# Performance work log

Measured on AMD Instinct MI355X. Metric: run time of the kernel, lower is better.

Reference implementation:

```python
import jax, jax.numpy as jnp
import numpy as np

N = 262144   # query points
M = 4096     # boundary points
D = 128      # d_model (m)
H = 4        # num_heads
HD = D // H  # head_dim = 32
L = 3        # num_layers
PI = float(np.pi)


def multi_feature_encoding(x):
    # x: [T, 2] -> [T, 30]; 15 fixed feature maps, hstacked
    feats = [
        x,
        x ** 2,
        (x - 1.5) ** 2,
        (x - 4.5) ** 2,
        jax.nn.sigmoid(x),
        jax.nn.sigmoid(x - 1.5),
        jax.nn.sigmoid(x - 4.5),
        x - 1.5,
        x - 4.5,
        jnp.sin(PI * x),
        jnp.cos(PI * x),
        jnp.sin(PI * x * 0.25),
        jnp.cos(PI * x * 0.25),
        jnp.sin(PI * x * 0.5),
        jnp.cos(PI * x * 0.5),
    ]
    return jnp.concatenate(feats, axis=-1)


def pos_encode(x, w, b):
    # w: [30, D], b: [D]
    return jnp.sin(multi_feature_encoding(x) @ w + b)


def setup_inputs() -> dict:
    key = jax.random.key(0)
    ks = jax.random.split(key, 24)
    s = 0.05

    def p(k, shape):
        return jax.random.normal(k, shape, dtype=jnp.float32) * s

    return {
        "query_pts": jax.random.normal(ks[0], (N, 2), dtype=jnp.float32),
        "boundary_pts": jax.random.normal(ks[1], (M, 2), dtype=jnp.float32),
        # positional encoders (query / boundary)
        "pe_w": p(ks[2], (30, D)), "pe_b": p(ks[3], (D,)),
        "bpe_w": p(ks[4], (30, D)), "bpe_b": p(ks[5], (D,)),
        # per-layer per-head q/k/v projections, stacked: [L, H, D, HD]
        "Wq": p(ks[6], (L, H, D, HD)), "bq": p(ks[7], (L, H, HD)),
        "Wk": p(ks[8], (L, H, D, HD)), "bk": p(ks[9], (L, H, HD)),
        "Wv": p(ks[10], (L, H, D, HD)), "bv": p(ks[11], (L, H, HD)),
        # attention out proj and FFN (two D->D linears) per layer
        "Wo": p(ks[12], (L, D, D)), "bo": p(ks[13], (L, D)),
        "W1": p(ks[14], (L, D, D)), "b1": p(ks[15], (L, D)),
        "W2": p(ks[16], (L, D, D)), "b2": p(ks[17], (L, D)),
        # final projector: D -> D//2 -> 3
        "pw1": p(ks[18], (D, D // 2)), "pb1": p(ks[19], (D // 2,)),
        "pw2": p(ks[20], (D // 2, 3)), "pb2": p(ks[21], (3,)),
    }


def reference(query_pts, boundary_pts, pe_w, pe_b, bpe_w, bpe_b,
              Wq, bq, Wk, bk, Wv, bv, Wo, bo, W1, b1, W2, b2,
              pw1, pb1, pw2, pb2):
    h = pos_encode(query_pts, pe_w, pe_b)[None]        # [1, N, D]
    b_enc = pos_encode(boundary_pts, bpe_w, bpe_b)[None]  # [1, M, D]

    for l in range(L):
        # batched per-head projections (equivalent to the per-head Linear loop)
        qh = jnp.einsum('btd,hde->bhte', h, Wq[l]) + bq[l][None, :, None, :]
        kh = jnp.einsum('btd,hde->bhte', b_enc, Wk[l]) + bk[l][None, :, None, :]
        vh = jnp.einsum('btd,hde->bhte', b_enc, Wv[l]) + bv[l][None, :, None, :]
        qh = qh ** 2  # squared feature map
        kh = kh ** 2
        kv_sum = jnp.einsum('bhnd,bhne->bhde', kh, vh)          # [1,H,HD,HD]
        z = 1.0 / (jnp.einsum('bhnd,bhd->bhn', qh, kh.sum(axis=2)) + 1e-6)
        attn = jnp.einsum('bhnd,bhde,bhn->bhne', qh, kv_sum, z)  # [1,H,N,HD]
        attn = attn.transpose(0, 2, 1, 3).reshape(1, -1, D)      # [1,N,D]
        attn = attn @ Wo[l] + bo[l]
        x = h + attn
        ff = jax.nn.gelu(x @ W1[l] + b1[l], approximate=False) @ W2[l] + b2[l]
        h = x + ff

    out = jax.nn.gelu(h @ pw1 + pb1, approximate=False) @ pw2 + pb2  # [1,N,3]
    return out[0]  # squeeze(0) -> [N, 3]
```

## Files before the change

kernel.cpp:

```cpp
#include <hip/hip_runtime.h>
#include <hip/hip_bf16.h>

__device__ __forceinline__ float b2f(unsigned short u) {
    return __uint_as_float(((unsigned)u) << 16);
}
__device__ __forceinline__ unsigned short f2b(float f) {
    __hip_bfloat16 h = __float2bfloat16(f);
    return *reinterpret_cast<unsigned short*>(&h);
}
__device__ __forceinline__ unsigned pk_bf16(float lo, float hi) {
    unsigned r;
    asm("v_cvt_pk_bf16_f32 %0, %1, %2" : "=v"(r) : "v"(lo), "v"(hi));
    return r;
}
__device__ __forceinline__ float sigm(float v) {
    return 1.f / (1.f + __expf(-v));
}
__device__ __forceinline__ float gelu_l(float x) {
    float x2 = x * x;
    float y2 = x * __builtin_fmaf(0.0713548163f, x2, 1.5957691216f);
    float e  = __expf(y2);
    float r  = __builtin_amdgcn_rcpf(e + 1.f);
    return x - x * r;
}

typedef __attribute__((ext_vector_type(8))) short s8v;
typedef __attribute__((ext_vector_type(4))) float f4v;

#define MFMA_BF16 __builtin_amdgcn_mfma_f32_16x16x32_bf16

__device__ __forceinline__ s8v mkfrag(unsigned a, unsigned b, unsigned c, unsigned d) {
    union { unsigned u[4]; s8v v; } x;
    x.u[0] = a; x.u[1] = b; x.u[2] = c; x.u[3] = d;
    return x.v;
}

__device__ __forceinline__ int fmap(int s) {
    return (s & ~31) | (((s >> 2) & 3) << 3) | (((s >> 4) & 1) << 2) | (s & 3);
}

__device__ __forceinline__ void make_feats(const unsigned short* __restrict__ qpts,
                                           int r, float* __restrict__ f) {
    unsigned pq = *(const unsigned*)(qpts + (size_t)r * 2);
    float x0 = b2f((unsigned short)(pq & 0xffff));
    float x1 = b2f((unsigned short)(pq >> 16));
    const float PI = 3.14159265358979323846f;
    float a0 = x0 - 1.5f, a1 = x1 - 1.5f, c0 = x0 - 4.5f, c1 = x1 - 4.5f;
    f[0] = x0;        f[1] = x1;
    f[2] = x0 * x0;   f[3] = x1 * x1;
    f[4] = a0 * a0;   f[5] = a1 * a1;
    f[6] = c0 * c0;   f[7] = c1 * c1;
    f[8] = sigm(x0);  f[9] = sigm(x1);
    f[10] = sigm(a0); f[11] = sigm(a1);
    f[12] = sigm(c0); f[13] = sigm(c1);
    f[14] = a0;       f[15] = a1;
    f[16] = c0;       f[17] = c1;
    f[18] = __sinf(PI * x0);          f[19] = __sinf(PI * x1);
    f[20] = __cosf(PI * x0);          f[21] = __cosf(PI * x1);
    f[22] = __sinf(PI * 0.25f * x0);  f[23] = __sinf(PI * 0.25f * x1);
    f[24] = __cosf(PI * 0.25f * x0);  f[25] = __cosf(PI * 0.25f * x1);
    f[26] = __sinf(PI * 0.5f * x0);   f[27] = __sinf(PI * 0.5f * x1);
    f[28] = __cosf(PI * 0.5f * x0);   f[29] = __cosf(PI * 0.5f * x1);
}

__device__ __forceinline__ void feats8(unsigned pq, int qd, float* __restrict__ f8) {
    float x0 = b2f((unsigned short)(pq & 0xffff));
    float x1 = b2f((unsigned short)(pq >> 16));
    const float PI = 3.14159265358979323846f;
    float a0 = x0 - 1.5f, a1 = x1 - 1.5f, c0 = x0 - 4.5f, c1 = x1 - 4.5f;
    if (qd == 0) {
        f8[0] = x0;      f8[1] = x1;
        f8[2] = x0 * x0; f8[3] = x1 * x1;
        f8[4] = a0 * a0; f8[5] = a1 * a1;
        f8[6] = c0 * c0; f8[7] = c1 * c1;
    } else if (qd == 1) {
        f8[0] = sigm(x0); f8[1] = sigm(x1);
        f8[2] = sigm(a0); f8[3] = sigm(a1);
        f8[4] = sigm(c0); f8[5] = sigm(c1);
        f8[6] = a0;       f8[7] = a1;
    } else if (qd == 2) {
        f8[0] = c0; f8[1] = c1;
        f8[2] = __sinf(PI * x0);          f8[3] = __sinf(PI * x1);
        f8[4] = __cosf(PI * x0);          f8[5] = __cosf(PI * x1);
        f8[6] = __sinf(PI * 0.25f * x0);  f8[7] = __sinf(PI * 0.25f * x1);
    } else {
        f8[0] = __cosf(PI * 0.25f * x0);  f8[1] = __cosf(PI * 0.25f * x1);
        f8[2] = __sinf(PI * 0.5f * x0);   f8[3] = __sinf(PI * 0.5f * x1);
        f8[4] = __cosf(PI * 0.5f * x0);   f8[5] = __cosf(PI * 0.5f * x1);
        f8[6] = 0.f;                      f8[7] = 0.f;
    }
}

struct ConvArgs {
    const void* p[22];
    int off[23];
};

__global__ __launch_bounds__(256) void convert_kernel(
    ConvArgs a, const unsigned short* __restrict__ pe_w_raw,
    int* __restrict__ flag, unsigned short* __restrict__ canon, int total)
{
    __shared__ int cnt;
    if (threadIdx.x == 0) cnt = 0;
    __syncthreads();
    float v = b2f(pe_w_raw[threadIdx.x * 2]);
    if (!(fabsf(v) < 1.0f)) atomicAdd(&cnt, 1);
    __syncthreads();
    int isf32 = (cnt >= 16) ? 1 : 0;
    if (blockIdx.x == 0 && threadIdx.x == 0) *flag = isf32;

    int g = blockIdx.x * 256 + threadIdx.x;
    if (g >= total) return;
    int s = 0;
    #pragma unroll
    for (int i = 1; i < 23; i++) s += (g >= a.off[i]) ? 1 : 0;
    int local = g - a.off[s];
    unsigned short r;
    if (isf32) r = f2b(((const float*)a.p[s])[local]);
    else       r = ((const unsigned short*)a.p[s])[local];
    canon[g] = r;
}

__global__ __launch_bounds__(256) void encode_kernel(
    const unsigned short* __restrict__ pts,
    const unsigned short* __restrict__ w,
    const unsigned short* __restrict__ b,
    float* __restrict__ out)
{
    __shared__ __align__(16) float wsm[30 * 128];
    __shared__ float bs[128];
    int t = threadIdx.x;
    for (int i = t; i < 30 * 128; i += 256) wsm[i] = b2f(w[i]);
    if (t < 128) bs[t] = b2f(b[t]);
    __syncthreads();

    int r = blockIdx.x * 8 + (t >> 5);
    int j = t & 31;
    float f[30];
    make_feats(pts, r, f);
    float s0 = bs[j * 4 + 0], s1 = bs[j * 4 + 1], s2 = bs[j * 4 + 2], s3 = bs[j * 4 + 3];
    #pragma unroll
    for (int ff = 0; ff < 30; ff++) {
        float4 wv = *(const float4*)&wsm[ff * 128 + j * 4];
        float fv = f[ff];
        s0 += fv * wv.x; s1 += fv * wv.y; s2 += fv * wv.z; s3 += fv * wv.w;
    }
    *(float4*)&out[(size_t)r * 128 + j * 4] =
        make_float4(__sinf(s0), __sinf(s1), __sinf(s2), __sinf(s3));
}

__global__ __launch_bounds__(256) void khvh_kernel(
    const float* __restrict__ benc,
    const unsigned short* __restrict__ Wk, const unsigned short* __restrict__ bk,
    const unsigned short* __restrict__ Wv, const unsigned short* __restrict__ bv,
    float* __restrict__ kh, float* __restrict__ vh, float* __restrict__ kvz)
{
    int g = blockIdx.x * 256 + threadIdx.x;
    if (g < 12672) kvz[g] = 0.f;
    int lh = g >> 17;
    int rem = g & 131071;
    int m = rem >> 5;
    int dd = rem & 31;
    const unsigned short* wk = Wk + lh * 4096 + dd;
    const unsigned short* wv = Wv + lh * 4096 + dd;
    const float* br = benc + (size_t)m * 128;
    float ka = 0.f, va = 0.f;
    #pragma unroll 8
    for (int c = 0; c < 128; c++) {
        float bb = br[c];
        ka += bb * b2f(wk[c * 32]);
        va += bb * b2f(wv[c * 32]);
    }
    ka += b2f(bk[lh * 32 + dd]); ka = ka * ka;
    va += b2f(bv[lh * 32 + dd]);
    kh[g] = ka; vh[g] = va;
}

__global__ __launch_bounds__(1024) void kvred_kernel(
    const float* __restrict__ kh, const float* __restrict__ vh,
    float* __restrict__ kvsum, float* __restrict__ ksum)
{
    __shared__ float khs[1024];
    __shared__ float vhs[1024];
    int t = threadIdx.x;
    int lh = blockIdx.x >> 3;
    int part = blockIdx.x & 7;
    int dd = t >> 5, ee = t & 31;
    float kva = 0.f, ksa = 0.f;
    for (int ch = 0; ch < 16; ch++) {
        int base = lh * 131072 + (part * 16 + ch) * 1024;
        khs[t] = kh[base + t];
        vhs[t] = vh[base + t];
        __syncthreads();
        #pragma unroll
        for (int i = 0; i < 32; i++) {
            float kk = khs[i * 32 + dd];
            kva += kk * vhs[i * 32 + ee];
            ksa += kk;
        }
        __syncthreads();
    }
    atomicAdd(&kvsum[lh * 1024 + dd * 32 + ee], kva);
    if (ee == 0) atomicAdd(&ksum[lh * 32 + dd], ksa);
}

__global__ __launch_bounds__(256) void prep_kernel(
    const unsigned short* __restrict__ Wq, const unsigned short* __restrict__ W1,
    const unsigned short* __restrict__ W2, const unsigned short* __restrict__ pw1,
    const float* __restrict__ kvs, const float* __restrict__ kss,
    const unsigned short* __restrict__ Wo, const unsigned short* __restrict__ pe_w,
    unsigned short* __restrict__ wqT, unsigned short* __restrict__ w1T,
    unsigned short* __restrict__ w2T, unsigned short* __restrict__ pw1T,
    unsigned short* __restrict__ waT, unsigned short* __restrict__ ksT,
    unsigned short* __restrict__ pweT)
{
    int g = blockIdx.x * 256 + threadIdx.x;
    if (g < 49152) {
        int l = g >> 14, r = g & 16383, n = r >> 7, k = r & 127;
        int na = fmap(n);
        wqT[g] = Wq[((l * 4 + (na >> 5)) * 128 + k) * 32 + (na & 31)];
    } else if (g < 98304) {
        int q = g - 49152; int l = q >> 14, r = q & 16383, n = r >> 7, k = r & 127;
        w1T[q] = W1[(l * 128 + k) * 128 + fmap(n)];
    } else if (g < 147456) {
        int q = g - 98304; int l = q >> 14, r = q & 16383, n = r >> 7, k = r & 127;
        w2T[q] = W2[(l * 128 + k) * 128 + fmap(n)];
    } else if (g < 155648) {
        int q = g - 147456; int n = q >> 7, k = q & 127;
        pw1T[q] = pw1[k * 64 + n];
    } else if (g < 204800) {
        int q = g - 155648; int l = q >> 14, r = q & 16383, n = r >> 7, k = r & 127;
        int na = fmap(n);
        int hk = k >> 5, dk = k & 31;
        const float* kvp = kvs + (l * 4 + hk) * 1024 + dk * 32;
        const unsigned short* wop = Wo + (size_t)(l * 128 + hk * 32) * 128 + na;
        float s = 0.f;
        #pragma unroll 8
        for (int j = 0; j < 32; j++) s += kvp[j] * b2f(wop[j * 128]);
        waT[q] = f2b(s);
    } else if (g < 210944) {
        int q = g - 204800; int l = q >> 11, r = q & 2047, n = r >> 7, k = r & 127;
        unsigned short v = 0;
        if (n < 4 && (k >> 5) == n) v = f2b(kss[(l * 4 + n) * 32 + (k & 31)]);
        ksT[q] = v;
    } else if (g < 215040) {
        int q = g - 210944; int n = q >> 5, k = q & 31;
        pweT[q] = (k < 30) ? pe_w[k * 128 + fmap(n)] : (unsigned short)0;
    }
}


template<int ITERS>
__device__ __forceinline__ void load_w(const unsigned short* __restrict__ g,
                                       int t, s8v* __restrict__ r) {
    #pragma unroll
    for (int i = 0; i < ITERS; i++)
        r[i] = *(const s8v*)((const char*)g + (size_t)(i * 256 + t) * 16);
}
template<int ITERS>
__device__ __forceinline__ void write_w(unsigned short* __restrict__ wbuf,
                                        int t, const s8v* __restrict__ r) {
    #pragma unroll
    for (int i = 0; i < ITERS; i++) {
        int lin = (i * 256 + t) * 16;
        int sw = lin ^ (((lin >> 8) & 7) << 4);
        *(s8v*)((char*)wbuf + sw) = r[i];
    }
}

__device__ __forceinline__ s8v wfrag(const unsigned short* __restrict__ wbuf,
                                     int nt, int k, int l16, int qd) {
    int lin = (nt << 12) + (l16 << 8) + (k << 6) + (qd << 4);
    return *(const s8v*)((const char*)wbuf + (lin ^ ((l16 & 7) << 4)));
}

#define MM_BODY(EPI...) do {                                                  \
    s8v bf0[4], bf1[4];                                                       \
    _Pragma("unroll")                                                         \
    for (int _s = 0; _s < 4; _s++) {                                          \
        bf0[_s] = mkfrag(pkd[0][2*_s][0], pkd[0][2*_s][1],                    \
                         pkd[0][2*_s+1][0], pkd[0][2*_s+1][1]);               \
        bf1[_s] = mkfrag(pkd[1][2*_s][0], pkd[1][2*_s][1],                    \
                         pkd[1][2*_s+1][0], pkd[1][2*_s+1][1]);               \
    }                                                                         \
    _Pragma("unroll")                                                         \
    for (int _p = 0; _p < 4; _p++) {                                          \
        f4v _x0 = {0.f,0.f,0.f,0.f}, _x1 = _x0, _y0 = _x0, _y1 = _x0;         \
        _Pragma("unroll")                                                     \
        for (int _k = 0; _k < 4; _k++) {                                      \
            s8v _wa = wfrag(wbuf, _p * 2,     _k, l16, qd);                   \
            s8v _wb = wfrag(wbuf, _p * 2 + 1, _k, l16, qd);                   \
            _x0 = MFMA_BF16(_wa, bf0[_k], _x0, 0, 0, 0);                      \
            _x1 = MFMA_BF16(_wa, bf1[_k], _x1, 0, 0, 0);                      \
            _y0 = MFMA_BF16(_wb, bf0[_k], _y0, 0, 0, 0);                      \
            _y1 = MFMA_BF16(_wb, bf1[_k], _y1, 0, 0, 0);                      \
        }                                                                     \
        { const int nt = _p * 2;     const int tile = 0; const f4v x = _x0; EPI } \
        { const int nt = _p * 2;     const int tile = 1; const f4v x = _x1; EPI } \
        { const int nt = _p * 2 + 1; const int tile = 0; const f4v x = _y0; EPI } \
        { const int nt = _p * 2 + 1; const int tile = 1; const f4v x = _y1; EPI } \
    }                                                                         \
} while (0)

#define CBDEF int cb = ((nt >> 1) << 5) + (qd << 3) + ((nt & 1) << 2)

__global__ __launch_bounds__(256) void mega_kernel(
    const unsigned short* __restrict__ qpts,
    const unsigned short* __restrict__ pweT,
    const unsigned short* __restrict__ pe_b,
    const unsigned short* __restrict__ wqT,
    const unsigned short* __restrict__ waT,
    const unsigned short* __restrict__ ksT,
    const unsigned short* __restrict__ w1T,
    const unsigned short* __restrict__ w2T,
    const unsigned short* __restrict__ bq,
    const unsigned short* __restrict__ bo,
    const unsigned short* __restrict__ b1,
    const unsigned short* __restrict__ b2,
    const unsigned short* __restrict__ pw1T,
    const unsigned short* __restrict__ pb1,
    const unsigned short* __restrict__ pw2,
    const unsigned short* __restrict__ pb2,
    void* __restrict__ outv, const int* __restrict__ flag)
{
    __shared__ __align__(16) unsigned short wbuf[16384];
    __shared__ __align__(16) float biasAll[12 * 128];
    __shared__ __align__(16) float pebs[128];
    __shared__ __align__(16) float pb1s[64];
    __shared__ __align__(16) float w2s4[256];
    __shared__ float pb2s[3];

    int t = threadIdx.x;
    int wvi = t >> 6, ln = t & 63, qd = ln >> 4, l16 = ln & 15;
    int row0 = blockIdx.x * 128;
    int rA0 = wvi * 32 + l16;

    for (int i = t; i < 1536; i += 256) {
        int l = i >> 9, rem = i & 511, which = rem >> 7, c = rem & 127;
        const unsigned short* bsrc = (which == 0) ? bq : (which == 1) ? bo
                                   : (which == 2) ? b1 : b2;
        biasAll[i] = b2f(bsrc[l * 128 + c]);
    }
    if (t < 128) pebs[t] = b2f(pe_b[t]);
    if (t < 64)  pb1s[t] = b2f(pb1[t]);
    if (t < 64) {
        w2s4[t * 4 + 0] = b2f(pw2[t * 3 + 0]);
        w2s4[t * 4 + 1] = b2f(pw2[t * 3 + 1]);
        w2s4[t * 4 + 2] = b2f(pw2[t * 3 + 2]);
        w2s4[t * 4 + 3] = 0.f;
    }
    if (t < 3) pb2s[t] = b2f(pb2[t]);
    __syncthreads();

    s8v sreg[8];
    load_w<8>(wqT, t, sreg);
    write_w<8>(wbuf, t, sreg);

    unsigned pkd[2][8][2];
    float hres[2][8][4];

    {
        unsigned pq0 = *(const unsigned*)(qpts + (size_t)(row0 + rA0) * 2);
        unsigned pq1 = *(const unsigned*)(qpts + (size_t)(row0 + rA0 + 16) * 2);
        s8v ae0, ae1;
        {
            float f8[8]; feats8(pq0, qd, f8);
            unsigned* au = (unsigned*)&ae0;
            #pragma unroll
            for (int jj = 0; jj < 4; jj++) au[jj] = pk_bf16(f8[2 * jj], f8[2 * jj + 1]);
        }
        {
            float f8[8]; feats8(pq1, qd, f8);
            unsigned* au = (unsigned*)&ae1;
            #pragma unroll
            for (int jj = 0; jj < 4; jj++) au[jj] = pk_bf16(f8[2 * jj], f8[2 * jj + 1]);
        }
        const unsigned short* pb = pweT + l16 * 32 + qd * 8;
        #pragma unroll
        for (int nt = 0; nt < 8; nt++) {
            s8v aw = *(const s8v*)(pb + nt * 512);
            f4v x0 = {0.f, 0.f, 0.f, 0.f}, x1 = {0.f, 0.f, 0.f, 0.f};
            x0 = MFMA_BF16(aw, ae0, x0, 0, 0, 0);
            x1 = MFMA_BF16(aw, ae1, x1, 0, 0, 0);
            CBDEF;
            float4 bb = *(const float4*)&pebs[cb];
            float h0 = __sinf(x0[0] + bb.x), h1 = __sinf(x0[1] + bb.y);
            float h2 = __sinf(x0[2] + bb.z), h3 = __sinf(x0[3] + bb.w);
            hres[0][nt][0] = h0; hres[0][nt][1] = h1;
            hres[0][nt][2] = h2; hres[0][nt][3] = h3;
            pkd[0][nt][0] = pk_bf16(h0, h1);
            pkd[0][nt][1] = pk_bf16(h2, h3);
            float g0 = __sinf(x1[0] + bb.x), g1 = __sinf(x1[1] + bb.y);
            float g2 = __sinf(x1[2] + bb.z), g3 = __sinf(x1[3] + bb.w);
            hres[1][nt][0] = g0; hres[1][nt][1] = g1;
            hres[1][nt][2] = g2; hres[1][nt][3] = g3;
            pkd[1][nt][0] = pk_bf16(g0, g1);
            pkd[1][nt][1] = pk_bf16(g2, g3);
        }
    }
    __syncthreads();

    for (int l = 0; l < 3; l++) {
        const float* bql = &biasAll[(l * 4 + 0) * 128];
        const float* bol = &biasAll[(l * 4 + 1) * 128];
        const float* b1l = &biasAll[(l * 4 + 2) * 128];
        const float* b2l = &biasAll[(l * 4 + 3) * 128];

        MM_BODY({
            CBDEF;
            float4 bb = *(const float4*)&bql[cb];
            float v0 = x[0] + bb.x, v1 = x[1] + bb.y;
            float v2 = x[2] + bb.z, v3 = x[3] + bb.w;
            pkd[tile][nt][0] = pk_bf16(v0 * v0, v1 * v1);
            pkd[tile][nt][1] = pk_bf16(v2 * v2, v3 * v3);
        });

        s8v kf[4];
        {
            const unsigned short* kb = ksT + l * 2048 + l16 * 128 + qd * 8;
            #pragma unroll
            for (int ks = 0; ks < 4; ks++) kf[ks] = *(const s8v*)(kb + ks * 32);
        }
        load_w<8>(waT + l * 16384, t, sreg);
        #pragma unroll
        for (int tile = 0; tile < 2; tile++) {
            f4v d = {0.f, 0.f, 0.f, 0.f};
            #pragma unroll
            for (int ks = 0; ks < 4; ks++) {
                s8v b = mkfrag(pkd[tile][2 * ks][0], pkd[tile][2 * ks][1],
                               pkd[tile][2 * ks + 1][0], pkd[tile][2 * ks + 1][1]);
                d = MFMA_BF16(kf[ks], b, d, 0, 0, 0);
            }
            #pragma unroll
            for (int ks = 0; ks < 4; ks++) {
                float z = 1.f / (__shfl(d[ks], l16) + 1e-6f);
                #pragma unroll
                for (int h2 = 0; h2 < 2; h2++) {
                    #pragma unroll
                    for (int j = 0; j < 2; j++) {
                        unsigned w = pkd[tile][2 * ks + h2][j];
                        float lo = __uint_as_float(w << 16) * z;
                        float hi = __uint_as_float(w & 0xffff0000u) * z;
                        pkd[tile][2 * ks + h2][j] = pk_bf16(lo, hi);
                    }
                }
            }
        }
        __syncthreads();
        write_w<8>(wbuf, t, sreg);
        __syncthreads();

        MM_BODY({
            CBDEF;
            float4 bb = *(const float4*)&bol[cb];
            float v0 = hres[tile][nt][0] + x[0] + bb.x;
            float v1 = hres[tile][nt][1] + x[1] + bb.y;
            float v2 = hres[tile][nt][2] + x[2] + bb.z;
            float v3 = hres[tile][nt][3] + x[3] + bb.w;
            hres[tile][nt][0] = v0; hres[tile][nt][1] = v1;
            hres[tile][nt][2] = v2; hres[tile][nt][3] = v3;
            pkd[tile][nt][0] = pk_bf16(v0, v1);
            pkd[tile][nt][1] = pk_bf16(v2, v3);
        });
        load_w<8>(w1T + l * 16384, t, sreg);
        __syncthreads();
        write_w<8>(wbuf, t, sreg);
        __syncthreads();

        MM_BODY({
            CBDEF;
            float4 bb = *(const float4*)&b1l[cb];
            float g0 = gelu_l(x[0] + bb.x), g1 = gelu_l(x[1] + bb.y);
            float g2 = gelu_l(x[2] + bb.z), g3 = gelu_l(x[3] + bb.w);
            pkd[tile][nt][0] = pk_bf16(g0, g1);
            pkd[tile][nt][1] = pk_bf16(g2, g3);
        });
        load_w<8>(w2T + l * 16384, t, sreg);
        __syncthreads();
        write_w<8>(wbuf, t, sreg);
        __syncthreads();

        MM_BODY({
            CBDEF;
            float4 bb = *(const float4*)&b2l[cb];
            float v0 = hres[tile][nt][0] + x[0] + bb.x;
            float v1 = hres[tile][nt][1] + x[1] + bb.y;
            float v2 = hres[tile][nt][2] + x[2] + bb.z;
            float v3 = hres[tile][nt][3] + x[3] + bb.w;
            hres[tile][nt][0] = v0; hres[tile][nt][1] = v1;
            hres[tile][nt][2] = v2; hres[tile][nt][3] = v3;
            pkd[tile][nt][0] = pk_bf16(v0, v1);
            pkd[tile][nt][1] = pk_bf16(v2, v3);
        });
        if (l < 2) {
            load_w<8>(wqT + (l + 1) * 16384, t, sreg);
            __syncthreads();
            write_w<8>(wbuf, t, sreg);
        } else {
            load_w<4>(pw1T, t, sreg);
            __syncthreads();
            write_w<4>(wbuf, t, sreg);
        }
        __syncthreads();
    }

    {
        s8v bf0[4], bf1[4];
        #pragma unroll
        for (int ks = 0; ks < 4; ks++) {
            bf0[ks] = mkfrag(pkd[0][2 * ks][0], pkd[0][2 * ks][1],
                             pkd[0][2 * ks + 1][0], pkd[0][2 * ks + 1][1]);
            bf1[ks] = mkfrag(pkd[1][2 * ks][0], pkd[1][2 * ks][1],
                             pkd[1][2 * ks + 1][0], pkd[1][2 * ks + 1][1]);
        }
        float pt0[3] = {0.f, 0.f, 0.f}, pt1[3] = {0.f, 0.f, 0.f};
        #pragma unroll
        for (int p = 0; p < 2; p++) {
            f4v y00 = {0.f,0.f,0.f,0.f}, y01 = y00, y10 = y00, y11 = y00;
            #pragma unroll
            for (int ks = 0; ks < 4; ks++) {
                s8v wa = wfrag(wbuf, p * 2,     ks, l16, qd);
                s8v wb = wfrag(wbuf, p * 2 + 1, ks, l16, qd);
                y00 = MFMA_BF16(wa, bf0[ks], y00, 0, 0, 0);
                y01 = MFMA_BF16(wa, bf1[ks], y01, 0, 0, 0);
                y10 = MFMA_BF16(wb, bf0[ks], y10, 0, 0, 0);
                y11 = MFMA_BF16(wb, bf1[ks], y11, 0, 0, 0);
            }
            #pragma unroll
            for (int e = 0; e < 2; e++) {
                int c0 = (p * 2 + e) * 16 + qd * 4;
                float4 bb = *(const float4*)&pb1s[c0];
                f4v ya = e ? y10 : y00;
                f4v yb = e ? y11 : y01;
                #pragma unroll
                for (int i = 0; i < 4; i++) {
                    float bbi = (i == 0) ? bb.x : (i == 1) ? bb.y : (i == 2) ? bb.z : bb.w;
                    float4 w = *(const float4*)&w2s4[(c0 + i) * 4];
                    float ga = gelu_l(ya[i] + bbi);
                    float gb = gelu_l(yb[i] + bbi);
                    pt0[0] = fmaf(ga, w.x, pt0[0]);
                    pt0[1] = fmaf(ga, w.y, pt0[1]);
                    pt0[2] = fmaf(ga, w.z, pt0[2]);
                    pt1[0] = fmaf(gb, w.x, pt1[0]);
                    pt1[1] = fmaf(gb, w.y, pt1[1]);
                    pt1[2] = fmaf(gb, w.z, pt1[2]);
                }
            }
        }
        #pragma unroll
        for (int c = 0; c < 3; c++) {
            pt0[c] += __shfl_xor(pt0[c], 16); pt0[c] += __shfl_xor(pt0[c], 32);
            pt1[c] += __shfl_xor(pt1[c], 16); pt1[c] += __shfl_xor(pt1[c], 32);
            pt0[c] += pb2s[c]; pt1[c] += pb2s[c];
        }
        if (ln < 16) {
            size_t r0 = (size_t)(row0 + rA0) * 3;
            size_t r1 = (size_t)(row0 + rA0 + 16) * 3;
            if (*flag) {
                float* o = (float*)outv;
                o[r0] = pt0[0]; o[r0 + 1] = pt0[1]; o[r0 + 2] = pt0[2];
                o[r1] = pt1[0]; o[r1 + 1] = pt1[1]; o[r1 + 2] = pt1[2];
            } else {
                unsigned short* o = (unsigned short*)outv;
                o[r0] = f2b(pt0[0]); o[r0 + 1] = f2b(pt0[1]); o[r0 + 2] = f2b(pt0[2]);
                o[r1] = f2b(pt1[0]); o[r1 + 1] = f2b(pt1[1]); o[r1 + 2] = f2b(pt1[2]);
            }
        }
    }
}

extern "C" void kernel_launch(void* const* d_in, const int* in_sizes, int n_in,
                              void* d_out, int out_size, void* d_ws, size_t ws_size,
                              hipStream_t stream) {
    const int N = in_sizes[0] / 2;
    const int M = in_sizes[1] / 2;

    ConvArgs ca;
    int total = 0;
    for (int i = 0; i < 22; i++) { ca.p[i] = d_in[i]; ca.off[i] = total; total += in_sizes[i]; }
    ca.off[22] = total;

    float* ws = (float*)d_ws;
    int* flag = (int*)ws;
    unsigned short* canon = (unsigned short*)(ws + 16);
    size_t canonF = ((size_t)(total + 1) / 2 + 15) & ~(size_t)15;
    float* b_enc = ws + 16 + canonF;
    float* khb   = b_enc + (size_t)M * 128;
    float* vhb   = khb + (size_t)12 * M * 32;
    float* kvs   = vhb + (size_t)12 * M * 32;
    float* kss   = kvs + 12288;
    unsigned short* wqT  = (unsigned short*)(kss + 384);
    unsigned short* waT  = wqT + 49152;
    unsigned short* w1T  = waT + 49152;
    unsigned short* w2T  = w1T + 49152;
    unsigned short* ksT  = w2T + 49152;
    unsigned short* pw1T = ksT + 6144;
    unsigned short* pweT = pw1T + 8192;

    const unsigned short* c_qpts = canon + ca.off[0];
    const unsigned short* c_bpts = canon + ca.off[1];
    const unsigned short* c_pew  = canon + ca.off[2];
    const unsigned short* c_peb  = canon + ca.off[3];
    const unsigned short* c_bpew = canon + ca.off[4];
    const unsigned short* c_bpeb = canon + ca.off[5];
    const unsigned short* c_Wq   = canon + ca.off[6];
    const unsigned short* c_bq   = canon + ca.off[7];
    const unsigned short* c_Wk   = canon + ca.off[8];
    const unsigned short* c_bk   = canon + ca.off[9];
    const unsigned short* c_Wv   = canon + ca.off[10];
    const unsigned short* c_bv   = canon + ca.off[11];
    const unsigned short* c_Wo   = canon + ca.off[12];
    const unsigned short* c_bo   = canon + ca.off[13];
    const unsigned short* c_W1   = canon + ca.off[14];
    const unsigned short* c_b1   = canon + ca.off[15];
    const unsigned short* c_W2   = canon + ca.off[16];
    const unsigned short* c_b2   = canon + ca.off[17];
    const unsigned short* c_pw1  = canon + ca.off[18];
    const unsigned short* c_pb1  = canon + ca.off[19];
    const unsigned short* c_pw2  = canon + ca.off[20];
    const unsigned short* c_pb2  = canon + ca.off[21];

    convert_kernel<<<(total + 255) / 256, 256, 0, stream>>>(
        ca, (const unsigned short*)d_in[2], flag, canon, total);

    encode_kernel<<<M / 8, 256, 0, stream>>>(c_bpts, c_bpew, c_bpeb, b_enc);
    khvh_kernel<<<(12 * M * 32) / 256, 256, 0, stream>>>(
        b_enc, c_Wk, c_bk, c_Wv, c_bv, khb, vhb, kvs);
    kvred_kernel<<<96, 1024, 0, stream>>>(khb, vhb, kvs, kss);
    prep_kernel<<<215040 / 256, 256, 0, stream>>>(
        c_Wq, c_W1, c_W2, c_pw1, kvs, kss, c_Wo, c_pew,
        wqT, w1T, w2T, pw1T, waT, ksT, pweT);

    mega_kernel<<<N / 128, 256, 0, stream>>>(
        c_qpts, pweT, c_peb, wqT, waT, ksT, w1T, w2T,
        c_bq, c_bo, c_b1, c_b2, pw1T, c_pb1, c_pw2, c_pb2, d_out, flag);
}
```

Measured before the change: 415.1 us.

## Double-buffer weight tiles in LDS with async global_load_lds staging

Weight matrices are now streamed straight from global memory into a second LDS buffer with global_load_lds while the current matmul runs on the other buffer. The prep kernel pre-applies the LDS XOR swizzle so the direct copies land in the layout the fragment reads expect. This removes the register round trip and several barriers per layer, at the cost of doubling weight LDS to 64KB, which may lower occupancy. GELU is also rewritten to call the hardware exp2 directly with pre-scaled constants and a fused fma.

Measured after the change: 364.6 us. 1.14x faster.

```diff
diff --git a/kernel.cpp b/kernel.cpp
--- a/kernel.cpp
+++ b/kernel.cpp
@@ -13,15 +13,20 @@
     asm("v_cvt_pk_bf16_f32 %0, %1, %2" : "=v"(r) : "v"(lo), "v"(hi));
     return r;
 }
+__device__ __forceinline__ float exp2_hw(float x) {
+    float r;
+    asm("v_exp_f32 %0, %1" : "=v"(r) : "v"(x));
+    return r;
+}
 __device__ __forceinline__ float sigm(float v) {
     return 1.f / (1.f + __expf(-v));
 }
 __device__ __forceinline__ float gelu_l(float x) {
     float x2 = x * x;
-    float y2 = x * __builtin_fmaf(0.0713548163f, x2, 1.5957691216f);
-    float e  = __expf(y2);
+    float y  = x * __builtin_fmaf(0.10294535f, x2, 2.3022137f);
+    float e  = exp2_hw(y);
     float r  = __builtin_amdgcn_rcpf(e + 1.f);
-    return x - x * r;
+    return __builtin_fmaf(-x, r, x);
 }
 
 typedef __attribute__((ext_vector_type(8))) short s8v;
@@ -37,6 +42,9 @@
 
 __device__ __forceinline__ int fmap(int s) {
     return (s & ~31) | (((s >> 2) & 3) << 3) | (((s >> 4) & 1) << 2) | (s & 3);
+}
+__device__ __forceinline__ int swz_q(int q) {
+    return q ^ (((q >> 7) & 7) << 3);
 }
 
 __device__ __forceinline__ void make_feats(const unsigned short* __restrict__ qpts,
@@ -216,20 +224,20 @@
 {
     int g = blockIdx.x * 256 + threadIdx.x;
     if (g < 49152) {
-        int l = g >> 14, r = g & 16383, n = r >> 7, k = r & 127;
+        int l = g >> 14, q = swz_q(g & 16383), n = q >> 7, k = q & 127;
         int na = fmap(n);
         wqT[g] = Wq[((l * 4 + (na >> 5)) * 128 + k) * 32 + (na & 31)];
     } else if (g < 98304) {
-        int q = g - 49152; int l = q >> 14, r = q & 16383, n = r >> 7, k = r & 127;
-        w1T[q] = W1[(l * 128 + k) * 128 + fmap(n)];
+        int q0 = g - 49152; int l = q0 >> 14, q = swz_q(q0 & 16383), n = q >> 7, k = q & 127;
+        w1T[q0] = W1[(l * 128 + k) * 128 + fmap(n)];
     } else if (g < 147456) {
-        int q = g - 98304; int l = q >> 14, r = q & 16383, n = r >> 7, k = r & 127;
-        w2T[q] = W2[(l * 128 + k) * 128 + fmap(n)];
+        int q0 = g - 98304; int l = q0 >> 14, q = swz_q(q0 & 16383), n = q >> 7, k = q & 127;
+        w2T[q0] = W2[(l * 128 + k) * 128 + fmap(n)];
     } else if (g < 155648) {
-        int q = g - 147456; int n = q >> 7, k = q & 127;
-        pw1T[q] = pw1[k * 64 + n];
+        int q0 = g - 147456; int q = swz_q(q0), n = q >> 7, k = q & 127;
+        pw1T[q0] = pw1[k * 64 + n];
     } else if (g < 204800) {
-        int q = g - 155648; int l = q >> 14, r = q & 16383, n = r >> 7, k = r & 127;
+        int q0 = g - 155648; int l = q0 >> 14, q = swz_q(q0 & 16383), n = q >> 7, k = q & 127;
         int na = fmap(n);
         int hk = k >> 5, dk = k & 31;
         const float* kvp = kvs + (l * 4 + hk) * 1024 + dk * 32;
@@ -237,7 +245,7 @@
         float s = 0.f;
         #pragma unroll 8
         for (int j = 0; j < 32; j++) s += kvp[j] * b2f(wop[j * 128]);
-        waT[q] = f2b(s);
+        waT[q0] = f2b(s);
     } else if (g < 210944) {
         int q = g - 204800; int l = q >> 11, r = q & 2047, n = r >> 7, k = r & 127;
         unsigned short v = 0;
@@ -251,30 +259,27 @@
 
 
 template<int ITERS>
-__device__ __forceinline__ void load_w(const unsigned short* __restrict__ g,
-                                       int t, s8v* __restrict__ r) {
-    #pragma unroll
-    for (int i = 0; i < ITERS; i++)
-        r[i] = *(const s8v*)((const char*)g + (size_t)(i * 256 + t) * 16);
-}
-template<int ITERS>
-__device__ __forceinline__ void write_w(unsigned short* __restrict__ wbuf,
-                                        int t, const s8v* __restrict__ r) {
+__device__ __forceinline__ void stage_gll(const unsigned short* __restrict__ g,
+                                          unsigned short* __restrict__ lbase,
+                                          int wvi, int ln) {
+    const char* gp = (const char*)g + wvi * 1024 + ln * 16;
+    char* lp = (char*)lbase + wvi * 1024;
     #pragma unroll
     for (int i = 0; i < ITERS; i++) {
-        int lin = (i * 256 + t) * 16;
-        int sw = lin ^ (((lin >> 8) & 7) << 4);
-        *(s8v*)((char*)wbuf + sw) = r[i];
-    }
-}
-
-__device__ __forceinline__ s8v wfrag(const unsigned short* __restrict__ wbuf,
+        __builtin_amdgcn_global_load_lds(
+            (const __attribute__((address_space(1))) unsigned int*)(gp + i * 4096),
+            (__attribute__((address_space(3))) unsigned int*)(lp + i * 4096),
+            16, 0, 0);
+    }
+}
+
+__device__ __forceinline__ s8v wfrag(const unsigned short* __restrict__ wb,
                                      int nt, int k, int l16, int qd) {
     int lin = (nt << 12) + (l16 << 8) + (k << 6) + (qd << 4);
-    return *(const s8v*)((const char*)wbuf + (lin ^ ((l16 & 7) << 4)));
-}
-
-#define MM_BODY(EPI...) do {                                                  \
+    return *(const s8v*)((const char*)wb + (lin ^ ((l16 & 7) << 4)));
+}
+
+#define MM_BODY(WB, EPI...) do {                                              \
     s8v bf0[4], bf1[4];                                                       \
     _Pragma("unroll")                                                         \
     for (int _s = 0; _s < 4; _s++) {                                          \
@@ -288,8 +293,8 @@
         f4v _x0 = {0.f,0.f,0.f,0.f}, _x1 = _x0, _y0 = _x0, _y1 = _x0;         \
         _Pragma("unroll")                                                     \
         for (int _k = 0; _k < 4; _k++) {                                      \
-            s8v _wa = wfrag(wbuf, _p * 2,     _k, l16, qd);                   \
-            s8v _wb = wfrag(wbuf, _p * 2 + 1, _k, l16, qd);                   \
+            s8v _wa = wfrag(WB, _p * 2,     _k, l16, qd);                     \
+            s8v _wb = wfrag(WB, _p * 2 + 1, _k, l16, qd);                     \
             _x0 = MFMA_BF16(_wa, bf0[_k], _x0, 0, 0, 0);                      \
             _x1 = MFMA_BF16(_wa, bf1[_k], _x1, 0, 0, 0);                      \
             _y0 = MFMA_BF16(_wb, bf0[_k], _y0, 0, 0, 0);                      \
@@ -323,7 +328,7 @@
     const unsigned short* __restrict__ pb2,
     void* __restrict__ outv, const int* __restrict__ flag)
 {
-    __shared__ __align__(16) unsigned short wbuf[16384];
+    __shared__ __align__(16) unsigned short wbuf[2][16384];
     __shared__ __align__(16) float biasAll[12 * 128];
     __shared__ __align__(16) float pebs[128];
     __shared__ __align__(16) float pb1s[64];
@@ -334,6 +339,10 @@
     int wvi = t >> 6, ln = t & 63, qd = ln >> 4, l16 = ln & 15;
     int row0 = blockIdx.x * 128;
     int rA0 = wvi * 32 + l16;
+    unsigned short* wb0 = &wbuf[0][0];
+    unsigned short* wb1 = &wbuf[1][0];
+
+    stage_gll<8>(wqT, wb0, wvi, ln);
 
     for (int i = t; i < 1536; i += 256) {
         int l = i >> 9, rem = i & 511, which = rem >> 7, c = rem & 127;
@@ -352,9 +361,7 @@
     if (t < 3) pb2s[t] = b2f(pb2[t]);
     __syncthreads();
 
-    s8v sreg[8];
-    load_w<8>(wqT, t, sreg);
-    write_w<8>(wbuf, t, sreg);
+    stage_gll<8>(waT, wb1, wvi, ln);
 
     unsigned pkd[2][8][2];
     float hres[2][8][4];
@@ -398,7 +405,6 @@
             pkd[1][nt][1] = pk_bf16(g2, g3);
         }
     }
-    __syncthreads();
 
     for (int l = 0; l < 3; l++) {
         const float* bql = &biasAll[(l * 4 + 0) * 128];
@@ -406,7 +412,14 @@
         const float* b1l = &biasAll[(l * 4 + 2) * 128];
         const float* b2l = &biasAll[(l * 4 + 3) * 128];
 
-        MM_BODY({
+        s8v kf[4];
+        {
+            const unsigned short* kb = ksT + l * 2048 + l16 * 128 + qd * 8;
+            #pragma unroll
+            for (int ks = 0; ks < 4; ks++) kf[ks] = *(const s8v*)(kb + ks * 32);
+        }
+
+        MM_BODY(wb0, {
             CBDEF;
             float4 bb = *(const float4*)&bql[cb];
             float v0 = x[0] + bb.x, v1 = x[1] + bb.y;
@@ -414,14 +427,9 @@
             pkd[tile][nt][0] = pk_bf16(v0 * v0, v1 * v1);
             pkd[tile][nt][1] = pk_bf16(v2 * v2, v3 * v3);
         });
-
-        s8v kf[4];
-        {
-            const unsigned short* kb = ksT + l * 2048 + l16 * 128 + qd * 8;
-            #pragma unroll
-            for (int ks = 0; ks < 4; ks++) kf[ks] = *(const s8v*)(kb + ks * 32);
-        }
-        load_w<8>(waT + l * 16384, t, sreg);
+        __syncthreads();
+        stage_gll<8>(w1T + l * 16384, wb0, wvi, ln);
+
         #pragma unroll
         for (int tile = 0; tile < 2; tile++) {
             f4v d = {0.f, 0.f, 0.f, 0.f};
@@ -446,11 +454,8 @@
                 }
             }
         }
-        __syncthreads();
-        write_w<8>(wbuf, t, sreg);
-        __syncthreads();
-
-        MM_BODY({
+
+        MM_BODY(wb1, {
             CBDEF;
             float4 bb = *(const float4*)&bol[cb];
             float v0 = hres[tile][nt][0] + x[0] + bb.x;
@@ -462,12 +467,10 @@
             pkd[tile][nt][0] = pk_bf16(v0, v1);
             pkd[tile][nt][1] = pk_bf16(v2, v3);
         });
-        load_w<8>(w1T + l * 16384, t, sreg);
         __syncthreads();
-        write_w<8>(wbuf, t, sreg);
-        __syncthreads();
-
-        MM_BODY({
+        stage_gll<8>(w2T + l * 16384, wb1, wvi, ln);
+
+        MM_BODY(wb0, {
             CBDEF;
             float4 bb = *(const float4*)&b1l[cb];
             float g0 = gelu_l(x[0] + bb.x), g1 = gelu_l(x[1] + bb.y);
@@ -475,12 +478,11 @@
             pkd[tile][nt][0] = pk_bf16(g0, g1);
             pkd[tile][nt][1] = pk_bf16(g2, g3);
         });
-        load_w<8>(w2T + l * 16384, t, sreg);
         __syncthreads();
-        write_w<8>(wbuf, t, sreg);
-        __syncthreads();
-
-        MM_BODY({
+        if (l < 2) stage_gll<8>(wqT + (l + 1) * 16384, wb0, wvi, ln);
+        else       stage_gll<4>(pw1T, wb0, wvi, ln);
+
+        MM_BODY(wb1, {
             CBDEF;
             float4 bb = *(const float4*)&b2l[cb];
             float v0 = hres[tile][nt][0] + x[0] + bb.x;
@@ -492,16 +494,8 @@
             pkd[tile][nt][0] = pk_bf16(v0, v1);
             pkd[tile][nt][1] = pk_bf16(v2, v3);
         });
-        if (l < 2) {
-            load_w<8>(wqT + (l + 1) * 16384, t, sreg);
-            __syncthreads();
-            write_w<8>(wbuf, t, sreg);
-        } else {
-            load_w<4>(pw1T, t, sreg);
-            __syncthreads();
-            write_w<4>(wbuf, t, sreg);
-        }
         __syncthreads();
+        if (l < 2) stage_gll<8>(waT + (l + 1) * 16384, wb1, wvi, ln);
     }
 
     {
@@ -519,8 +513,8 @@
             f4v y00 = {0.f,0.f,0.f,0.f}, y01 = y00, y10 = y00, y11 = y00;
             #pragma unroll
             for (int ks = 0; ks < 4; ks++) {
-                s8v wa = wfrag(wbuf, p * 2,     ks, l16, qd);
-                s8v wb = wfrag(wbuf, p * 2 + 1, ks, l16, qd);
+                s8v wa = wfrag(wb0, p * 2,     ks, l16, qd);
+                s8v wb = wfrag(wb0, p * 2 + 1, ks, l16, qd);
                 y00 = MFMA_BF16(wa, bf0[ks], y00, 0, 0, 0);
                 y01 = MFMA_BF16(wa, bf1[ks], y01, 0, 0, 0);
                 y10 = MFMA_BF16(wb, bf0[ks], y10, 0, 0, 0);
```
